# Performance work log

Measured on AMD Instinct MI355X. Metric: run time of the kernel, lower is better.

Reference implementation:

```python
import jax, jax.numpy as jnp
import numpy as np

E = 65536      # num edges
T = 262144     # num triplets
H = 128        # hidden_channels
D = 64         # int_emb_size
C = 8          # basis_emb_size
NR = 6         # num_radial
NS = 7         # num_spherical
NB = 6         # len(bt_list) = num_BT + 1
BT_LIST = (-1, 0, 1, 2, 3, 4)
NBS = 1        # num_before_skip (also used for after-skip list in original code)


def setup_inputs() -> dict:
    key = jax.random.key(0)
    ks = iter(jax.random.split(key, 40))
    s = 0.05
    p = lambda shape: jax.random.normal(next(ks), shape, dtype=jnp.float32) * s
    inp = dict(
        x=jax.random.normal(next(ks), (E, H), dtype=jnp.float32),
        rbf=jax.random.normal(next(ks), (E, NR), dtype=jnp.float32),
        sbf=jax.random.normal(next(ks), (T, NS * NR), dtype=jnp.float32),
        idx_kj=jax.random.randint(next(ks), (T,), 0, E),
        idx_ji=jax.random.randint(next(ks), (T,), 0, E),
        bt=jax.random.randint(next(ks), (E,), 0, 5),
        lambda_d=1,
        alpha=jnp.float32(0.7),
        # per-branch stacked weights (6 branches)
        W_kj=p((NB, H, H)), b_kj=jnp.zeros((NB, H), jnp.float32),
        W_rbf1=p((NB, NR, C)), W_rbf2=p((NB, C, H)),
        W_sbf1=p((NB, NS * NR, C)), W_sbf2=p((NB, C, D)),
        W_down=p((NB, H, D)),
        W_ji=p((H, H)), b_ji=jnp.zeros((H,), jnp.float32),
        W_up=p((D, H)),
        rb1_w=p((NBS, H, H)), rb1_b=jnp.zeros((NBS, H), jnp.float32),
        rb2_w=p((NBS, H, H)), rb2_b=jnp.zeros((NBS, H), jnp.float32),
        W_lin=p((H, H)), b_lin=jnp.zeros((H,), jnp.float32),
        ra1_w=p((NBS, H, H)), ra1_b=jnp.zeros((NBS, H), jnp.float32),
        ra2_w=p((NBS, H, H)), ra2_b=jnp.zeros((NBS, H), jnp.float32),
    )
    return inp


def reference(x, rbf, sbf, idx_kj, idx_ji, bt, lambda_d, alpha,
              W_kj, b_kj, W_rbf1, W_rbf2, W_sbf1, W_sbf2, W_down,
              W_ji, b_ji, W_up, rb1_w, rb1_b, rb2_w, rb2_b,
              W_lin, b_lin, ra1_w, ra1_b, ra2_w, ra2_b):
    act = jax.nn.silu

    x_ji = act(x @ W_ji + b_ji)                                  # [E,H]

    # per-branch edge transforms, vectorized over the 6 branches (axis b)
    tmp = act(jnp.einsum('eh,bhg->beg', x, W_kj) + b_kj[:, None, :])   # [B,E,H]
    rbf_p = jnp.einsum('er,brc->bec', rbf, W_rbf1)                     # [B,E,C]
    rbf_p = jnp.einsum('bec,bcg->beg', rbf_p, W_rbf2)                  # [B,E,H]
    tmp = tmp * rbf_p
    down = act(jnp.einsum('beh,bhd->bed', tmp, W_down))                # [B,E,D]

    sbf_p = jnp.einsum('ts,bsc->btc', sbf, W_sbf1)                     # [B,T,C]
    sbf_p = jnp.einsum('btc,bcd->btd', sbf_p, W_sbf2)                  # [B,T,D]

    spe = down[:, idx_kj, :] * sbf_p                                   # [B,T,D]

    # last branch scattered with weight alpha
    x_kj_tot = alpha * jax.ops.segment_sum(spe[-1], idx_ji, num_segments=E)

    # per band-type masked scatter with weight (1 - alpha)
    bt_trip = bt[idx_kj]                                               # [T]
    for b, btv in enumerate(BT_LIST):
        m = (bt_trip == btv).astype(x.dtype)[:, None]
        x_kj_tot = x_kj_tot + (1.0 - alpha) * jax.ops.segment_sum(
            spe[b] * m, idx_ji, num_segments=E)

    x_kj = act(x_kj_tot @ W_up)                                        # [E,H]
    h = x_ji + x_kj
    for i in range(rb1_w.shape[0]):
        h = h + act(act(h @ rb1_w[i] + rb1_b[i]) @ rb2_w[i] + rb2_b[i])
    h = act(h @ W_lin + b_lin) + x
    for i in range(ra1_w.shape[0]):
        h = h + act(act(h @ ra1_w[i] + ra1_b[i]) @ ra2_w[i] + ra2_b[i])
    return h
```

## Files before the change

### kernel.cpp

```cpp
#include <hip/hip_runtime.h>
#include <hip/hip_bf16.h>
#include <stdint.h>

typedef __bf16 bf16_t;
typedef bf16_t bf16x8 __attribute__((ext_vector_type(8)));
typedef bf16_t bf16x2 __attribute__((ext_vector_type(2)));
typedef float f32x4 __attribute__((ext_vector_type(4)));

#define E_N 65536
#define T_N 262144
#define CAP 16
#define OVF_MAX T_N

__device__ __forceinline__ float silu_f(float v) {
  return v / (1.0f + __expf(-v));
}

__device__ __forceinline__ int permrow(int n) {
  return (n & ~31) | ((n & 1) << 4) | ((n & 30) >> 1);
}

__device__ __forceinline__ uint32_t pack_bf16(float a, float b) {
  union { bf16x2 h; uint32_t u; } u;
  u.h[0] = (bf16_t)a; u.h[1] = (bf16_t)b;
  return u.u;
}

__device__ __forceinline__ void g2l16(const void* g, void* l) {
  __builtin_amdgcn_global_load_lds(
      (const __attribute__((address_space(1))) void*)g,
      (__attribute__((address_space(3))) void*)l, 16, 0, 0);
}

template<int KI, int NTJ>
__device__ __forceinline__ void gemm_tile(const bf16_t* A, const bf16_t* B,
                                          int mb, int nb, int l16, int q,
                                          f32x4 (&acc)[2][NTJ]) {
#pragma unroll
  for (int kt = 0; kt < KI; ++kt) {
    const int sw = ((kt * 4 + q) ^ l16) << 3;
    bf16x8 a0 = *(const bf16x8*)(A + ((mb + l16) << 7) + sw);
    bf16x8 a1 = *(const bf16x8*)(A + ((mb + 16 + l16) << 7) + sw);
#pragma unroll
    for (int tj = 0; tj < NTJ; ++tj) {
      bf16x8 b = *(const bf16x8*)(B + ((nb + tj * 16 + l16) << 7) + sw);
      acc[0][tj] = __builtin_amdgcn_mfma_f32_16x16x32_bf16(a0, b, acc[0][tj], 0, 0, 0);
      acc[1][tj] = __builtin_amdgcn_mfma_f32_16x16x32_bf16(a1, b, acc[1][tj], 0, 0, 0);
    }
  }
}

template<int C4>
__device__ __forceinline__ void stage_x(bf16_t* dst, const float* src, int tid) {
  const float4* g = (const float4*)src;
#pragma unroll
  for (int i = tid; i < 64 * C4; i += 256) {
    const int row = i / C4, c4 = i % C4;
    float4 v = g[i];
    bf16_t t[4] = {(bf16_t)v.x, (bf16_t)v.y, (bf16_t)v.z, (bf16_t)v.w};
    *(uint2*)(dst + (row << 7) + ((((c4 >> 1) ^ (row & 15)) << 3) | ((c4 & 1) << 2))) =
        *(const uint2*)t;
  }
}

__global__ __launch_bounds__(256, 4)
void prep_c8_kernel(
    const float* __restrict__ W_ji, const float* __restrict__ W_kj,
    const float* __restrict__ W_down, const float* __restrict__ W_up,
    const float* __restrict__ rb1, const float* __restrict__ rb2,
    const float* __restrict__ W_lin, const float* __restrict__ ra1,
    const float* __restrict__ ra2, const float* __restrict__ W_rbf1,
    const float* __restrict__ W_rbf2, const float* __restrict__ x,
    char* __restrict__ wm_img, char* __restrict__ wdn_img,
    char* __restrict__ pset, bf16_t* __restrict__ wcb,
    bf16_t* __restrict__ ximg,
    const float* __restrict__ sbf, const int* __restrict__ idx_kj,
    const int* __restrict__ idx_ji, const int* __restrict__ bt,
    const float* __restrict__ Wsbf1,
    float* __restrict__ c8g, uint32_t* __restrict__ meta,
    int* __restrict__ cnt, int* __restrict__ list,
    int* __restrict__ ovf)
{
  __shared__ __align__(16) union {
    bf16_t tile[64 * 128];
    struct {
      float s_sbf[64 * 44];
      float s_W1[2016];
      float s_c8[64 * 16];
      int s_bs[64];
    } c;
  } S;

  const int tid = threadIdx.x;
  const int blk = blockIdx.x;

  if (blk < 4096) {
    const int base = blk * 64;

    for (int i = tid; i < 2016; i += 256) S.c.s_W1[i] = Wsbf1[i];
    if (tid < 64) {
      const int t = base + tid;
      const int kj = idx_kj[t];
      const int ji = idx_ji[t];
      const int bs = bt[kj] + 1;
      S.c.s_bs[tid] = bs;
      meta[t] = (uint32_t)kj | ((uint32_t)bs << 16);
      const int pos = atomicAdd(&cnt[ji], 1);
      if (pos < CAP) {
        list[ji * CAP + pos] = t;
      } else {
        const int o = atomicAdd(&ovf[0], 1);
        if (o < OVF_MAX) { ovf[2 + 2 * o] = t; ovf[2 + 2 * o + 1] = ji; }
      }
    }
    {
      const float2* sg = (const float2*)(sbf + (size_t)base * 42);
      for (int i = tid; i < 64 * 21; i += 256) {
        const int r = i / 21, c2 = i - r * 21;
        const float2 v = sg[i];
        S.c.s_sbf[r * 44 + c2 * 2] = v.x;
        S.c.s_sbf[r * 44 + c2 * 2 + 1] = v.y;
      }
    }
    __syncthreads();

    {
      const int i = tid >> 2;
      const int brr = (tid >> 1) & 1;
      const int cg = tid & 1;
      const int b = brr ? S.c.s_bs[i] : 5;
      const float* w = &S.c.s_W1[b * 336 + cg * 4];
      const float* sb = &S.c.s_sbf[i * 44];
      float a0 = 0.f, a1 = 0.f, a2 = 0.f, a3 = 0.f;
#pragma unroll
      for (int s = 0; s < 42; ++s) {
        const float sv = sb[s];
        const float* ws = w + s * 8;
        a0 += sv * ws[0]; a1 += sv * ws[1]; a2 += sv * ws[2]; a3 += sv * ws[3];
      }
      float* dc = &S.c.s_c8[i * 16 + brr * 8 + cg * 4];
      dc[0] = a0; dc[1] = a1; dc[2] = a2; dc[3] = a3;
    }
    __syncthreads();

    {
      const float4* s4 = (const float4*)S.c.s_c8;
      float4* g4 = (float4*)(c8g + (size_t)base * 16);
      g4[tid] = s4[tid];
    }
    return;
  }

  const int pblk = blk - 4096;
  if (pblk >= 115) {
    const int t = pblk - 115;
    stage_x<32>(S.tile, x + (size_t)t * 8192, tid);
    __syncthreads();
    uint4* dst = (uint4*)(ximg + (size_t)t * 8192);
    const uint4* s = (const uint4*)S.tile;
#pragma unroll
    for (int i = 0; i < 4; ++i) dst[i * 256 + tid] = s[i * 256 + tid];
    return;
  }
  if (pblk >= 112) {
    const int o = (pblk - 112) * 256 + tid;
    if (o < 640) {
      const int b = o >> 7, n = o & 127;
      bf16_t t[8];
#pragma unroll
      for (int r = 0; r < 6; ++r) {
        const float* w1 = W_rbf1 + (b + 1) * 48 + r * 8;
        const float* w2 = W_rbf2 + (b + 1) * 1024 + n;
        float s = 0.f;
#pragma unroll
        for (int c = 0; c < 8; ++c) s += w1[c] * w2[c * 128];
        t[r] = (bf16_t)s;
      }
      t[6] = (bf16_t)0.f; t[7] = (bf16_t)0.f;
      *(uint4*)(wcb + (b * 128 + n) * 8) = *(const uint4*)t;
    }
    return;
  }
  if (pblk >= 108) {
    const int item = (pblk - 108) * 256 + tid;
    const int n = item >> 3, k8 = item & 7;
    bf16_t t[8];
#pragma unroll
    for (int j = 0; j < 8; ++j) t[j] = (bf16_t)W_up[(k8 * 8 + j) * 128 + n];
    const int row = permrow(n);
    *(uint4*)((bf16_t*)pset + (row << 7) + ((k8 ^ (row & 15)) << 3)) = *(const uint4*)t;
    return;
  }
  if (pblk >= 88) {
    const int item = (pblk - 88) * 256 + tid;
    const int m = item >> 10, w = item & 1023;
    const int n = w >> 4, k8 = w & 15;
    const float* src = W_down + (m + 1) * 8192;
    bf16_t* img = (bf16_t*)(wdn_img + m * 16384);
    bf16_t t[8];
#pragma unroll
    for (int j = 0; j < 8; ++j) t[j] = (bf16_t)src[(k8 * 8 + j) * 64 + n];
    const int row = permrow(n);
    *(uint4*)(img + (row << 7) + ((k8 ^ (row & 15)) << 3)) = *(const uint4*)t;
    return;
  }
  const int item = pblk * 256 + tid;
  const int m = item >> 11, w = item & 2047;
  const int n = w >> 4, k8 = w & 15;
  const float* src; char* img;
  if (m == 0)      { src = W_ji;             img = wm_img; }
  else if (m <= 5) { src = W_kj + m * 16384; img = wm_img + m * 32768; }
  else if (m == 6) { src = rb1;   img = pset + 1 * 32768; }
  else if (m == 7) { src = rb2;   img = pset + 2 * 32768; }
  else if (m == 8) { src = W_lin; img = pset + 3 * 32768; }
  else if (m == 9) { src = ra1;   img = pset + 4 * 32768; }
  else             { src = ra2;   img = pset + 5 * 32768; }
  bf16_t t[8];
#pragma unroll
  for (int j = 0; j < 8; ++j) t[j] = (bf16_t)src[(k8 * 8 + j) * 128 + n];
  const int row = permrow(n);
  *(uint4*)((bf16_t*)img + (row << 7) + ((k8 ^ (row & 15)) << 3)) = *(const uint4*)t;
}

__global__ __launch_bounds__(256, 3)
void edge_kernel(const bf16_t* __restrict__ ximg, const float* __restrict__ rbf,
                 const float* __restrict__ b_kj, const float* __restrict__ b_ji,
                 const char* __restrict__ wm_img, const char* __restrict__ wdn_img,
                 const bf16_t* __restrict__ wcb,
                 bf16_t* __restrict__ x_ji_out, bf16_t* __restrict__ down)
{
  __shared__ __align__(16) bf16_t xA[64 * 128];
  __shared__ __align__(16) bf16_t Wb[128 * 128];
  __shared__ __align__(16) bf16_t wcbS[128 * 8];
  __shared__ __align__(16) bf16_t rbfS[64 * 8];
  __shared__ float biasS[128];

  const int tid = threadIdx.x;
  const int lane = tid & 63, wv = tid >> 6;
  const int q = lane >> 4, l16 = lane & 15;
  const int mb = (wv >> 1) * 32, nb = (wv & 1) * 64;
  const int eb = blockIdx.x;
  const int br = eb % 6;
  const int tile = eb / 6;
  const int R = tile * 64;

  {
    const char* xs = (const char*)(ximg + (size_t)tile * 8192);
    char* xd = (char*)xA;
#pragma unroll
    for (int c = 0; c < 4; ++c) {
      const int off = (c * 4 + wv) * 1024 + lane * 16;
      g2l16(xs + off, xd + off);
    }
    const char* wsrc = wm_img + (size_t)br * 32768;
    char* wd = (char*)Wb;
#pragma unroll
    for (int c = 0; c < 8; ++c) {
      const int off = (c * 4 + wv) * 1024 + lane * 16;
      g2l16(wsrc + off, wd + off);
    }
  }
  if (br == 0) {
    if (tid < 128) biasS[tid] = b_ji[tid];
  } else {
    if (tid < 128) biasS[tid] = b_kj[br * 128 + tid];
    if (wv < 2) {
      const char* cs = (const char*)(wcb + (size_t)(br - 1) * 1024);
      const int off = wv * 1024 + lane * 16;
      g2l16(cs + off, (char*)wcbS + off);
    }
    if (tid < 64) {
      const float* rg = rbf + (size_t)(R + tid) * 6;
      bf16_t t[8] = {(bf16_t)rg[0], (bf16_t)rg[1], (bf16_t)rg[2],
                     (bf16_t)rg[3], (bf16_t)rg[4], (bf16_t)rg[5],
                     (bf16_t)0.f, (bf16_t)0.f};
      *(uint4*)(rbfS + tid * 8) = *(const uint4*)t;
    }
  }
  __syncthreads();

  f32x4 acc[2][4] = {};
  gemm_tile<4, 4>(xA, Wb, mb, nb, l16, q, acc);

  if (br == 0) {
#pragma unroll
    for (int ti = 0; ti < 2; ++ti)
#pragma unroll
      for (int r = 0; r < 4; ++r) {
        const int row = mb + ti * 16 + q * 4 + r;
#pragma unroll
        for (int gl = 0; gl < 2; ++gl) {
          const int col0 = nb + gl * 32 + 2 * l16;
          const float2 b2 = *(const float2*)&biasS[col0];
          *(uint32_t*)&x_ji_out[(size_t)(R + row) * 128 + col0] =
              pack_bf16(silu_f(acc[ti][2 * gl][r] + b2.x),
                        silu_f(acc[ti][2 * gl + 1][r] + b2.y));
        }
      }
    return;
  }

  __syncthreads();

  {
    const char* ds = wdn_img + (size_t)(br - 1) * 16384;
    char* dd = (char*)Wb;
#pragma unroll
    for (int c = 0; c < 4; ++c) {
      const int off = (c * 4 + wv) * 1024 + lane * 16;
      g2l16(ds + off, dd + off);
    }
  }

  float wc[2][2][6];
#pragma unroll
  for (int gl = 0; gl < 2; ++gl)
#pragma unroll
    for (int j = 0; j < 2; ++j) {
      const int col = nb + gl * 32 + 2 * l16 + j;
      bf16x8 w8 = *(const bf16x8*)&wcbS[col * 8];
#pragma unroll
      for (int c = 0; c < 6; ++c) wc[gl][j][c] = (float)w8[c];
    }
#pragma unroll
  for (int ti = 0; ti < 2; ++ti)
#pragma unroll
    for (int r = 0; r < 4; ++r) {
      const int row = mb + ti * 16 + q * 4 + r;
      bf16x8 rv8 = *(const bf16x8*)&rbfS[row * 8];
      float rv[6];
#pragma unroll
      for (int c = 0; c < 6; ++c) rv[c] = (float)rv8[c];
#pragma unroll
      for (int gl = 0; gl < 2; ++gl) {
        const int col0 = nb + gl * 32 + 2 * l16;
        const float2 b2 = *(const float2*)&biasS[col0];
        float p0 = 0.f, p1 = 0.f;
#pragma unroll
        for (int c = 0; c < 6; ++c) {
          p0 += rv[c] * wc[gl][0][c];
          p1 += rv[c] * wc[gl][1][c];
        }
        const float v0 = silu_f(acc[ti][2 * gl][r] + b2.x) * p0;
        const float v1 = silu_f(acc[ti][2 * gl + 1][r] + b2.y) * p1;
        *(uint32_t*)&xA[(row << 7) + ((((col0 >> 3) ^ (row & 15)) << 3) | (col0 & 7))] =
            pack_bf16(v0, v1);
      }
    }
  __syncthreads();

  const int nb2 = (wv & 1) * 32;
  f32x4 acc2[2][2] = {};
  gemm_tile<4, 2>(xA, Wb, mb, nb2, l16, q, acc2);
#pragma unroll
  for (int ti = 0; ti < 2; ++ti)
#pragma unroll
    for (int r = 0; r < 4; ++r) {
      const int row = mb + ti * 16 + q * 4 + r;
      const int col0 = nb2 + 2 * l16;
      *(uint32_t*)&down[((size_t)(br - 1) * E_N + R + row) * 64 + col0] =
          pack_bf16(silu_f(acc2[ti][0][r]), silu_f(acc2[ti][1][r]));
    }
}

__global__ __launch_bounds__(256, 3)
void epi_kernel(const float* __restrict__ x, const bf16_t* __restrict__ x_ji,
                const char* __restrict__ pset,
                const int* __restrict__ cnt, const int* __restrict__ list,
                const uint32_t* __restrict__ meta, const float* __restrict__ c8g,
                const float* __restrict__ Wsbf2, const bf16_t* __restrict__ down,
                const float* __restrict__ alpha_p, const int* __restrict__ ovf,
                const float* __restrict__ rb1_b, const float* __restrict__ rb2_b,
                const float* __restrict__ lin_b, const float* __restrict__ ra1_b,
                const float* __restrict__ ra2_b,
                float* __restrict__ out)
{
  __shared__ __align__(16) bf16_t buf[64 * 128];
  __shared__ __align__(16) bf16_t Wb[128 * 128];
  __shared__ float biasS[2][128];

  const int tid = threadIdx.x;
  const int lane = tid & 63, wv = tid >> 6;
  const int q = lane >> 4, l16 = lane & 15;
  const int mb = (wv >> 1) * 32, nb = (wv & 1) * 64;
  const int R = blockIdx.x * 64;

#define DMA_W(SLOT) do {                                                         \
    const char* ps_ = pset + (size_t)(SLOT) * 32768;                             \
    char* wd_ = (char*)Wb;                                                       \
    _Pragma("unroll")                                                            \
    for (int c_ = 0; c_ < 8; ++c_) {                                             \
      const int off_ = (c_ * 4 + wv) * 1024 + lane * 16;                         \
      g2l16(ps_ + off_, wd_ + off_);                                             \
    }                                                                            \
  } while (0)

  DMA_W(0);

  {
    const int j = lane;
    const float alpha = alpha_p[0], oma = 1.f - alpha;
    float w5r[8];
#pragma unroll
    for (int c = 0; c < 8; ++c) w5r[c] = Wsbf2[5 * 512 + c * 64 + j];
    const int oc = ovf[0];

    for (int ee = 0; ee < 16; ++ee) {
      const int row = wv * 16 + ee;
      const int e = R + row;
      int n = cnt[e];
      if (n > CAP) n = CAP;
      int tk = 0; uint32_t mk = 0;
      if ((j & 15) < n) {
        tk = list[e * CAP + (j & 15)];
        mk = meta[tk];
      }
      float acc = 0.f;
      for (int k = 0; k < n; ++k) {
        const int t = __builtin_amdgcn_readfirstlane(__shfl(tk, k, 64));
        const uint32_t m = __builtin_amdgcn_readfirstlane(__shfl(mk, k, 64));
        const int kj = m & 0xffff;
        const int b  = m >> 16;
        const float g5 = (float)down[((size_t)4 * E_N + kj) * 64 + j];
        const float gb = (float)down[((size_t)(b - 1) * E_N + kj) * 64 + j];
        const float* cp = c8g + (size_t)t * 16;
        float d5 = 0.f, db = 0.f;
#pragma unroll
        for (int c = 0; c < 8; ++c) {
          d5 += cp[c]     * w5r[c];
          db += cp[8 + c] * Wsbf2[b * 512 + c * 64 + j];
        }
        acc += alpha * g5 * d5 + oma * gb * db;
      }
      for (int k = 0; k < oc; ++k) {
        const int ji = ovf[2 + 2 * k + 1];
        if (ji != e) continue;
        const int t = ovf[2 + 2 * k];
        const uint32_t m = meta[t];
        const int kj = m & 0xffff;
        const int b  = m >> 16;
        const float g5 = (float)down[((size_t)4 * E_N + kj) * 64 + j];
        const float gb = (float)down[((size_t)(b - 1) * E_N + kj) * 64 + j];
        const float* cp = c8g + (size_t)t * 16;
        float d5 = 0.f, db = 0.f;
#pragma unroll
        for (int c = 0; c < 8; ++c) {
          d5 += cp[c]     * w5r[c];
          db += cp[8 + c] * Wsbf2[b * 512 + c * 64 + j];
        }
        acc += alpha * g5 * d5 + oma * gb * db;
      }
      buf[(row << 7) + ((((j >> 3) ^ (row & 15)) << 3) | (j & 7))] = (bf16_t)acc;
    }
  }
  __syncthreads();

  f32x4 hreg[2][4];
  {
    f32x4 acc[2][4] = {};
    gemm_tile<2, 4>(buf, Wb, mb, nb, l16, q, acc);
    __syncthreads();
#pragma unroll
    for (int ti = 0; ti < 2; ++ti)
#pragma unroll
      for (int r = 0; r < 4; ++r) {
        const int row = mb + ti * 16 + q * 4 + r;
#pragma unroll
        for (int gl = 0; gl < 2; ++gl) {
          const int col0 = nb + gl * 32 + 2 * l16;
          union { uint32_t u; bf16x2 h; } xj;
          xj.u = *(const uint32_t*)&x_ji[(size_t)(R + row) * 128 + col0];
          const float h0 = (float)xj.h[0] + silu_f(acc[ti][2 * gl][r]);
          const float h1 = (float)xj.h[1] + silu_f(acc[ti][2 * gl + 1][r]);
          hreg[ti][2 * gl][r] = h0;
          hreg[ti][2 * gl + 1][r] = h1;
          *(uint32_t*)&buf[(row << 7) + ((((col0 >> 3) ^ (row & 15)) << 3) | (col0 & 7))] =
              pack_bf16(h0, h1);
        }
      }
    DMA_W(1);
    if (tid < 128) biasS[0][tid] = rb1_b[tid];
    __syncthreads();
  }

#define EPI_STAGE(K, NEXTSLOT, NEXTBIAS, BODY)                                   \
  {                                                                              \
    f32x4 acc[2][4] = {};                                                        \
    gemm_tile<4, 4>(buf, Wb, mb, nb, l16, q, acc);                               \
    __syncthreads();                                                             \
    const float* bs_ = biasS[((K) - 1) & 1];                                     \
    _Pragma("unroll")                                                            \
    for (int ti = 0; ti < 2; ++ti)                                               \
      _Pragma("unroll")                                                          \
      for (int r = 0; r < 4; ++r) {                                              \
        const int row = mb + ti * 16 + q * 4 + r;                                \
        _Pragma("unroll")                                                        \
        for (int gl = 0; gl < 2; ++gl) {                                         \
          const int col0 = nb + gl * 32 + 2 * l16;                               \
          const float2 b2 = *(const float2*)&bs_[col0];                          \
          const float g0 = acc[ti][2 * gl][r] + b2.x;                            \
          const float g1 = acc[ti][2 * gl + 1][r] + b2.y;                        \
          BODY                                                                   \
        }                                                                        \
      }                                                                          \
    if ((K) < 5) {                                                               \
      DMA_W(NEXTSLOT);                                                           \
      if (tid < 128) biasS[(K) & 1][tid] = NEXTBIAS[tid];                        \
      __syncthreads();                                                           \
    }                                                                            \
  }

  EPI_STAGE(1, 2, rb2_b, {
    *(uint32_t*)&buf[(row << 7) + ((((col0 >> 3) ^ (row & 15)) << 3) | (col0 & 7))] =
        pack_bf16(silu_f(g0), silu_f(g1));
  })

  EPI_STAGE(2, 3, lin_b, {
    const float h0 = hreg[ti][2 * gl][r] + silu_f(g0);
    const float h1 = hreg[ti][2 * gl + 1][r] + silu_f(g1);
    hreg[ti][2 * gl][r] = h0; hreg[ti][2 * gl + 1][r] = h1;
    *(uint32_t*)&buf[(row << 7) + ((((col0 >> 3) ^ (row & 15)) << 3) | (col0 & 7))] =
        pack_bf16(h0, h1);
  })

  EPI_STAGE(3, 4, ra1_b, {
    const float2 xv = *(const float2*)&x[(size_t)(R + row) * 128 + col0];
    const float h0 = silu_f(g0) + xv.x;
    const float h1 = silu_f(g1) + xv.y;
    hreg[ti][2 * gl][r] = h0; hreg[ti][2 * gl + 1][r] = h1;
    *(uint32_t*)&buf[(row << 7) + ((((col0 >> 3) ^ (row & 15)) << 3) | (col0 & 7))] =
        pack_bf16(h0, h1);
  })

  EPI_STAGE(4, 5, ra2_b, {
    *(uint32_t*)&buf[(row << 7) + ((((col0 >> 3) ^ (row & 15)) << 3) | (col0 & 7))] =
        pack_bf16(silu_f(g0), silu_f(g1));
  })

  EPI_STAGE(5, 0, ra2_b, {
    float2 o;
    o.x = hreg[ti][2 * gl][r] + silu_f(g0);
    o.y = hreg[ti][2 * gl + 1][r] + silu_f(g1);
    *(float2*)&out[(size_t)(R + row) * 128 + col0] = o;
  })
#undef EPI_STAGE
#undef DMA_W
}

extern "C" void kernel_launch(void* const* d_in, const int* in_sizes, int n_in,
                              void* d_out, int out_size, void* d_ws, size_t ws_size,
                              hipStream_t stream)
{
  (void)in_sizes; (void)n_in; (void)out_size; (void)ws_size;
  const float* x      = (const float*)d_in[0];
  const float* rbf    = (const float*)d_in[1];
  const float* sbf    = (const float*)d_in[2];
  const int*   idx_kj = (const int*)d_in[3];
  const int*   idx_ji = (const int*)d_in[4];
  const int*   bt     = (const int*)d_in[5];
  const float* alpha  = (const float*)d_in[7];
  const float* W_kj   = (const float*)d_in[8];
  const float* b_kj   = (const float*)d_in[9];
  const float* W_rbf1 = (const float*)d_in[10];
  const float* W_rbf2 = (const float*)d_in[11];
  const float* W_sbf1 = (const float*)d_in[12];
  const float* W_sbf2 = (const float*)d_in[13];
  const float* W_down = (const float*)d_in[14];
  const float* W_ji   = (const float*)d_in[15];
  const float* b_ji   = (const float*)d_in[16];
  const float* W_up   = (const float*)d_in[17];
  const float* rb1_w  = (const float*)d_in[18];
  const float* rb1_b  = (const float*)d_in[19];
  const float* rb2_w  = (const float*)d_in[20];
  const float* rb2_b  = (const float*)d_in[21];
  const float* W_lin  = (const float*)d_in[22];
  const float* b_lin  = (const float*)d_in[23];
  const float* ra1_w  = (const float*)d_in[24];
  const float* ra1_b  = (const float*)d_in[25];
  const float* ra2_w  = (const float*)d_in[26];
  const float* ra2_b  = (const float*)d_in[27];

  char* ws = (char*)d_ws;
  bf16_t* down   = (bf16_t*)(ws);
  bf16_t* x_ji   = (bf16_t*)(ws + 41943040);
  bf16_t* ximg   = (bf16_t*)(ws + 58720256);
  char*   wm_img = ws + 75497472;
  char*   wdn_img= ws + 75694080;
  char*   pset   = ws + 75776000;
  bf16_t* wcb    = (bf16_t*)(ws + 75972608);
  float*    c8g  = (float*)   (ws + 75982848);
  uint32_t* meta = (uint32_t*)(ws + 92760064);
  int*      list = (int*)     (ws + 93808640);
  int*      cnt  = (int*)     (ws + 98002944);
  int*      ovf  = (int*)     (ws + 98265088);

  hipMemsetAsync(cnt, 0, 262144 + 8, stream);
  prep_c8_kernel<<<5235, 256, 0, stream>>>(W_ji, W_kj, W_down, W_up, rb1_w,
                                           rb2_w, W_lin, ra1_w, ra2_w, W_rbf1,
                                           W_rbf2, x, wm_img, wdn_img, pset,
                                           wcb, ximg, sbf, idx_kj, idx_ji, bt,
                                           W_sbf1, c8g, meta, cnt, list, ovf);
  edge_kernel<<<E_N / 64 * 6, 256, 0, stream>>>(ximg, rbf, b_kj, b_ji, wm_img,
                                                wdn_img, wcb, x_ji, down);
  epi_kernel<<<E_N / 64, 256, 0, stream>>>(x, x_ji, pset, cnt, list, meta,
                                           c8g, W_sbf2, down, alpha, ovf,
                                           rb1_b, rb2_b, b_lin, ra1_b, ra2_b,
                                           (float*)d_out);
}
```

Measured before the change: 387.3 us.

## Split triplet gather into separate high-occupancy kernel feeding epilogue GEMMs

```diff
diff --git a/kernel.cpp b/kernel.cpp
--- a/kernel.cpp
+++ b/kernel.cpp
@@ -363,13 +363,86 @@
     }
 }
 
+__global__ __launch_bounds__(256, 8)
+void gather_kernel(const int* __restrict__ cnt, const int* __restrict__ list,
+                   const uint32_t* __restrict__ meta, const float* __restrict__ c8g,
+                   const float* __restrict__ Wsbf2, const bf16_t* __restrict__ down,
+                   const float* __restrict__ alpha_p, const int* __restrict__ ovf,
+                   float* __restrict__ xkj)
+{
+  __shared__ float sW2[3072];
+  for (int i = threadIdx.x; i < 3072; i += 256) sW2[i] = Wsbf2[i];
+  __syncthreads();
+
+  const int e = blockIdx.x * 4 + (threadIdx.x >> 6);
+  const int j = threadIdx.x & 63;
+  const float alpha = alpha_p[0], oma = 1.f - alpha;
+  const float* w5 = &sW2[5 * 512 + j];
+
+  int n = cnt[e];
+  if (n > CAP) n = CAP;
+
+  int tk = 0; uint32_t mk = 0;
+  if ((j & 15) < n) {
+    tk = list[e * CAP + (j & 15)];
+    mk = meta[tk];
+  }
+
+  float acc = 0.f;
+  const int nn = (n + 1) & ~1;
+  for (int k0 = 0; k0 < nn; k0 += 2) {
+    const int k1 = (k0 + 1 < n) ? k0 + 1 : n - 1;
+    const float sc1 = (k0 + 1 < n) ? 1.f : 0.f;
+    const int t0 = __builtin_amdgcn_readfirstlane(__shfl(tk, k0, 64));
+    const uint32_t m0 = __builtin_amdgcn_readfirstlane(__shfl(mk, k0, 64));
+    const int t1 = __builtin_amdgcn_readfirstlane(__shfl(tk, k1, 64));
+    const uint32_t m1 = __builtin_amdgcn_readfirstlane(__shfl(mk, k1, 64));
+    const int kj0 = m0 & 0xffff, b0 = m0 >> 16;
+    const int kj1 = m1 & 0xffff, b1 = m1 >> 16;
+    const float g5a = (float)down[((size_t)4 * E_N + kj0) * 64 + j];
+    const float gba = (float)down[((size_t)(b0 - 1) * E_N + kj0) * 64 + j];
+    const float g5b = (float)down[((size_t)4 * E_N + kj1) * 64 + j];
+    const float gbb = (float)down[((size_t)(b1 - 1) * E_N + kj1) * 64 + j];
+    const float* cp0 = c8g + (size_t)t0 * 16;
+    const float* cp1 = c8g + (size_t)t1 * 16;
+    float d5a = 0.f, dba = 0.f, d5b = 0.f, dbb = 0.f;
+#pragma unroll
+    for (int c = 0; c < 8; ++c) {
+      d5a += cp0[c]     * w5[c * 64];
+      dba += cp0[8 + c] * sW2[b0 * 512 + c * 64 + j];
+      d5b += cp1[c]     * w5[c * 64];
+      dbb += cp1[8 + c] * sW2[b1 * 512 + c * 64 + j];
+    }
+    acc += alpha * g5a * d5a + oma * gba * dba;
+    acc += sc1 * (alpha * g5b * d5b + oma * gbb * dbb);
+  }
+
+  const int oc = ovf[0];
+  for (int k = 0; k < oc; ++k) {
+    const int ji = ovf[2 + 2 * k + 1];
+    if (ji != e) continue;
+    const int t = ovf[2 + 2 * k];
+    const uint32_t m = meta[t];
+    const int kj = m & 0xffff;
+    const int b  = m >> 16;
+    const float g5 = (float)down[((size_t)4 * E_N + kj) * 64 + j];
+    const float gb = (float)down[((size_t)(b - 1) * E_N + kj) * 64 + j];
+    const float* cp = c8g + (size_t)t * 16;
+    float d5 = 0.f, db = 0.f;
+#pragma unroll
+    for (int c = 0; c < 8; ++c) {
+      d5 += cp[c]     * w5[c * 64];
+      db += cp[8 + c] * sW2[b * 512 + c * 64 + j];
+    }
+    acc += alpha * g5 * d5 + oma * gb * db;
+  }
+
+  xkj[(size_t)e * 64 + j] = acc;
+}
+
 __global__ __launch_bounds__(256, 3)
 void epi_kernel(const float* __restrict__ x, const bf16_t* __restrict__ x_ji,
-                const char* __restrict__ pset,
-                const int* __restrict__ cnt, const int* __restrict__ list,
-                const uint32_t* __restrict__ meta, const float* __restrict__ c8g,
-                const float* __restrict__ Wsbf2, const bf16_t* __restrict__ down,
-                const float* __restrict__ alpha_p, const int* __restrict__ ovf,
+                const float* __restrict__ xkj, const char* __restrict__ pset,
                 const float* __restrict__ rb1_b, const float* __restrict__ rb2_b,
                 const float* __restrict__ lin_b, const float* __restrict__ ra1_b,
                 const float* __restrict__ ra2_b,
@@ -395,64 +468,8 @@
     }                                                                            \
   } while (0)
 
+  stage_x<16>(buf, xkj + (size_t)R * 64, tid);
   DMA_W(0);
-
-  {
-    const int j = lane;
-    const float alpha = alpha_p[0], oma = 1.f - alpha;
-    float w5r[8];
-#pragma unroll
-    for (int c = 0; c < 8; ++c) w5r[c] = Wsbf2[5 * 512 + c * 64 + j];
-    const int oc = ovf[0];
-
-    for (int ee = 0; ee < 16; ++ee) {
-      const int row = wv * 16 + ee;
-      const int e = R + row;
-      int n = cnt[e];
-      if (n > CAP) n = CAP;
-      int tk = 0; uint32_t mk = 0;
-      if ((j & 15) < n) {
-        tk = list[e * CAP + (j & 15)];
-        mk = meta[tk];
-      }
-      float acc = 0.f;
-      for (int k = 0; k < n; ++k) {
-        const int t = __builtin_amdgcn_readfirstlane(__shfl(tk, k, 64));
-        const uint32_t m = __builtin_amdgcn_readfirstlane(__shfl(mk, k, 64));
-        const int kj = m & 0xffff;
-        const int b  = m >> 16;
-        const float g5 = (float)down[((size_t)4 * E_N + kj) * 64 + j];
-        const float gb = (float)down[((size_t)(b - 1) * E_N + kj) * 64 + j];
-        const float* cp = c8g + (size_t)t * 16;
-        float d5 = 0.f, db = 0.f;
-#pragma unroll
-        for (int c = 0; c < 8; ++c) {
-          d5 += cp[c]     * w5r[c];
-          db += cp[8 + c] * Wsbf2[b * 512 + c * 64 + j];
-        }
-        acc += alpha * g5 * d5 + oma * gb * db;
-      }
-      for (int k = 0; k < oc; ++k) {
-        const int ji = ovf[2 + 2 * k + 1];
-        if (ji != e) continue;
-        const int t = ovf[2 + 2 * k];
-        const uint32_t m = meta[t];
-        const int kj = m & 0xffff;
-        const int b  = m >> 16;
-        const float g5 = (float)down[((size_t)4 * E_N + kj) * 64 + j];
-        const float gb = (float)down[((size_t)(b - 1) * E_N + kj) * 64 + j];
-        const float* cp = c8g + (size_t)t * 16;
-        float d5 = 0.f, db = 0.f;
-#pragma unroll
-        for (int c = 0; c < 8; ++c) {
-          d5 += cp[c]     * w5r[c];
-          db += cp[8 + c] * Wsbf2[b * 512 + c * 64 + j];
-        }
-        acc += alpha * g5 * d5 + oma * gb * db;
-      }
-      buf[(row << 7) + ((((j >> 3) ^ (row & 15)) << 3) | (j & 7))] = (bf16_t)acc;
-    }
-  }
   __syncthreads();
 
   f32x4 hreg[2][4];
@@ -584,6 +601,7 @@
   bf16_t* down   = (bf16_t*)(ws);
   bf16_t* x_ji   = (bf16_t*)(ws + 41943040);
   bf16_t* ximg   = (bf16_t*)(ws + 58720256);
+  float*  xkj    = (float*) (ws + 58720256);
   char*   wm_img = ws + 75497472;
   char*   wdn_img= ws + 75694080;
   char*   pset   = ws + 75776000;
@@ -602,8 +620,9 @@
                                            W_sbf1, c8g, meta, cnt, list, ovf);
   edge_kernel<<<E_N / 64 * 6, 256, 0, stream>>>(ximg, rbf, b_kj, b_ji, wm_img,
                                                 wdn_img, wcb, x_ji, down);
-  epi_kernel<<<E_N / 64, 256, 0, stream>>>(x, x_ji, pset, cnt, list, meta,
-                                           c8g, W_sbf2, down, alpha, ovf,
+  gather_kernel<<<E_N / 4, 256, 0, stream>>>(cnt, list, meta, c8g, W_sbf2,
+                                             down, alpha, ovf, xkj);
+  epi_kernel<<<E_N / 64, 256, 0, stream>>>(x, x_ji, xkj, pset,
                                            rb1_b, rb2_b, b_lin, ra1_b, ra2_b,
                                            (float*)d_out);
 }
```

New measurement: 349.8 us. -9.7%, faster.
